# Optimization experiments

Measured on AMD Instinct MI355X. Metric: run time of the kernel, lower is better.

The kernel has to match this reference:

```python
import jax, jax.numpy as jnp
import numpy as np
import math

REG = 0.1      # entropic regularization (self.reg)
TEMP = 0.1     # self.temperature from kwargs
ITERS = 20     # self.iters
EPS = 1e-5     # torch LayerNorm eps
ALPHA_BOTH = -100.0


def _layernorm(t, g, b):
    mu = jnp.mean(t, axis=-1, keepdims=True)
    var = jnp.mean((t - mu) ** 2, axis=-1, keepdims=True)
    return (t - mu) / jnp.sqrt(var + EPS) * g + b


def setup_inputs() -> dict:
    key = jax.random.key(0)
    k1, k2, k3 = jax.random.split(key, 3)
    B, M, N, H = 2048, 36, 36, 768
    x = jax.random.normal(k1, (B, M, H), jnp.float32)
    y = jax.random.normal(k2, (B, N, H), jnp.float32)
    # dustbin scorer params: LayerNorm(H) -> Linear(H, 1)
    ln_g = jnp.ones((H,), jnp.float32)
    ln_b = jnp.zeros((H,), jnp.float32)
    w = jax.random.normal(k3, (H, 1), jnp.float32) * (1.0 / math.sqrt(H))
    b_lin = jnp.zeros((1,), jnp.float32)
    return {"x": x, "y": y, "ln_g": ln_g, "ln_b": ln_b, "w": w, "b_lin": b_lin}


def reference(x, y, ln_g, ln_b, w, b_lin):
    B, M, H = x.shape
    N = y.shape[1]
    # CosineScorer(temperature=1).score(x, y, get_diag=False)
    xn = x / jnp.linalg.norm(x, axis=-1, keepdims=True)
    yn = y / jnp.linalg.norm(y, axis=-1, keepdims=True)
    scores = jnp.einsum('bmh,bnh->bmn', xn, yn)            # (B, M, N)
    # tanh-clipped learned dustbin scores
    ax = jnp.tanh(_layernorm(x, ln_g, ln_b) @ w + b_lin)   # (B, M, 1)
    ay = jnp.tanh(_layernorm(y, ln_g, ln_b) @ w + b_lin)   # (B, N, 1)
    # augmented score matrix with dustbin row/col
    alpha_both = jnp.full((B, 1, 1), ALPHA_BOTH, scores.dtype)
    top = jnp.concatenate([scores, ax], axis=2)                       # (B, M, N+1)
    bot = jnp.concatenate([jnp.swapaxes(ay, 1, 2), alpha_both], axis=2)  # (B, 1, N+1)
    couplings = jnp.concatenate([top, bot], axis=1) / REG             # (B, M+1, N+1)
    # SuperGlue-style marginals: dustbins absorb the complementary mass
    norm_c = -math.log(M + N)
    log_mu = jnp.concatenate([jnp.full((M,), norm_c),
                              jnp.array([math.log(N) + norm_c])]).astype(scores.dtype)
    log_nu = jnp.concatenate([jnp.full((N,), norm_c),
                              jnp.array([math.log(M) + norm_c])]).astype(scores.dtype)

    def body(carry, _):
        u, v = carry
        u = log_mu[None, :] - jax.nn.logsumexp(couplings + v[:, None, :], axis=2)
        v = log_nu[None, :] - jax.nn.logsumexp(couplings + u[:, :, None], axis=1)
        return (u, v), None

    u0 = jnp.zeros((B, M + 1), scores.dtype)
    v0 = jnp.zeros((B, N + 1), scores.dtype)
    (u, v), _ = jax.lax.scan(body, (u0, v0), None, length=ITERS)
    Z = couplings + u[:, :, None] + v[:, None, :] - norm_c            # log matching, (B, M+1, N+1)
    # scalar alignment score per batch element: <P, S> / temperature
    total = jnp.sum(jnp.exp(Z[:, :-1, :-1]) * scores, axis=(1, 2)) / TEMP
    return Z, total
```

## Files before the change

kernel.cpp:

```cpp
#include <hip/hip_runtime.h>
#include <stdint.h>
#include <stddef.h>


typedef float  f4  __attribute__((ext_vector_type(4)));
typedef short  s8v __attribute__((ext_vector_type(8)));
typedef unsigned int u2v __attribute__((ext_vector_type(2)));

#define HD   768
#define MR   36
#define KC   128
#define NCH  6
#define AS   136
#define CS   44
#define LOG2E 1.4426950408889634f
#define LN2   0.6931471805599453f
#define L272  6.169925001442312f
#define KC2   (10.0f*LOG2E)
#define NEGB  (-1.0e30f)

__device__ __forceinline__ uint32_t pkbf2(float a, float b) {
    uint32_t ua = __float_as_uint(a), ub = __float_as_uint(b);
    ua += 0x7FFFu + ((ua >> 16) & 1u);
    ub += 0x7FFFu + ((ub >> 16) & 1u);
    return (ua >> 16) | (ub & 0xFFFF0000u);
}

__global__ __launch_bounds__(256, 3) void sinkhorn_kernel(
    const float* __restrict__ X, const float* __restrict__ Y,
    const float* __restrict__ LG, const float* __restrict__ LB,
    const float* __restrict__ W,  const float* __restrict__ BL,
    float* __restrict__ OUT, int NB)
{
    __shared__ __align__(16) uint16_t Al[48 * AS];
    __shared__ __align__(16) uint16_t Bt[48 * AS];
    __shared__ __align__(16) float C2 [37 * CS];
    __shared__ __align__(16) float C2T[37 * CS];
    __shared__ __align__(16) float u_l[40];
    __shared__ __align__(16) float v_l[40];
    __shared__ float stx[MR * 3], sty[MR * 3];
    __shared__ float rnx[MR], rny[MR];
    __shared__ float s_gw, s_bw, red[4];

    const int t  = threadIdx.x;
    const int b  = blockIdx.x;
    const int wv = t >> 6, ln = t & 63;
    const int c4 = t & 31, gg = t >> 5;

    if (t < 40) { u_l[t] = 0.0f; v_l[t] = 0.0f; }
    if (t < 37) {
        C2 [t * CS + 37] = NEGB; C2 [t * CS + 38] = NEGB; C2 [t * CS + 39] = NEGB;
        C2T[t * CS + 37] = NEGB; C2T[t * CS + 38] = NEGB; C2T[t * CS + 39] = NEGB;
    }
    if (wv == 3) {
        float a = 0.0f, c = 0.0f;
        for (int q = 0; q < 12; ++q) {
            int h = ln + 64 * q;
            float wval = W[h];
            a += LG[h] * wval; c += LB[h] * wval;
        }
        for (int o = 32; o > 0; o >>= 1) { a += __shfl_down(a, o); c += __shfl_down(c, o); }
        if (ln == 0) { s_gw = a; s_bw = c; }
    }

    float sx[5][3], sy[5][3];
    #pragma unroll
    for (int p = 0; p < 5; ++p)
        #pragma unroll
        for (int s = 0; s < 3; ++s) { sx[p][s] = 0.0f; sy[p][s] = 0.0f; }

    f4 acc[3];
    #pragma unroll
    for (int i = 0; i < 3; ++i) acc[i] = (f4){0.0f, 0.0f, 0.0f, 0.0f};

    const float* xb = X + (size_t)b * (MR * HD);
    const float* yb = Y + (size_t)b * (MR * HD);

    const int frow = ln & 15, fq = ln >> 4;
    const int rA = (wv * 16 + frow) * AS + fq * 8;

    for (int kc = 0; kc < NCH; ++kc) {
        const int k0 = kc * KC;
        f4 gv = *(const f4*)(LG + k0 + c4 * 4);
        f4 wvec = *(const f4*)(W + k0 + c4 * 4);
        f4 gw = gv * wvec;
        #pragma unroll
        for (int p = 0; p < 5; ++p) {
            if (p < 4 || t < 128) {
                const int row = (p < 4) ? (p * 8 + gg) : (32 + gg);
                f4 xv = *(const f4*)(xb + row * HD + k0 + c4 * 4);
                sx[p][0] += (xv.x + xv.y) + (xv.z + xv.w);
                sx[p][1] += xv.x * xv.x + xv.y * xv.y + xv.z * xv.z + xv.w * xv.w;
                sx[p][2] += xv.x * gw.x + xv.y * gw.y + xv.z * gw.z + xv.w * gw.w;
                u2v px; px.x = pkbf2(xv.x, xv.y); px.y = pkbf2(xv.z, xv.w);
                *(u2v*)&Al[row * AS + c4 * 4] = px;
                f4 yv = *(const f4*)(yb + row * HD + k0 + c4 * 4);
                sy[p][0] += (yv.x + yv.y) + (yv.z + yv.w);
                sy[p][1] += yv.x * yv.x + yv.y * yv.y + yv.z * yv.z + yv.w * yv.w;
                sy[p][2] += yv.x * gw.x + yv.y * gw.y + yv.z * gw.z + yv.w * gw.w;
                u2v py; py.x = pkbf2(yv.x, yv.y); py.y = pkbf2(yv.z, yv.w);
                *(u2v*)&Bt[row * AS + c4 * 4] = py;
            }
        }
        __syncthreads();
        if (wv < 3) {
            #pragma unroll
            for (int ks = 0; ks < 4; ++ks) {
                s8v af = *(const s8v*)&Al[rA + ks * 32];
                #pragma unroll
                for (int tn = 0; tn < 3; ++tn) {
                    s8v bf = *(const s8v*)&Bt[(tn * 16 + frow) * AS + fq * 8 + ks * 32];
                    acc[tn] = __builtin_amdgcn_mfma_f32_16x16x32_bf16(af, bf, acc[tn], 0, 0, 0);
                }
            }
        }
        __syncthreads();
    }

    #pragma unroll
    for (int p = 0; p < 5; ++p) {
        const int row = (p < 4) ? (p * 8 + gg) : (32 + gg);
        #pragma unroll
        for (int s = 0; s < 3; ++s) {
            float a = sx[p][s], c = sy[p][s];
            for (int o = 16; o > 0; o >>= 1) { a += __shfl_down(a, o, 32); c += __shfl_down(c, o, 32); }
            if ((t & 31) == 0 && row < MR) { stx[row * 3 + s] = a; sty[row * 3 + s] = c; }
        }
    }
    __syncthreads();

    {
        const float blin = BL[0];
        if (t < MR) {
            float Sx = stx[t * 3], Sxx = stx[t * 3 + 1], Sxw = stx[t * 3 + 2];
            rnx[t] = __builtin_amdgcn_rsqf(Sxx);
            float mu  = Sx * (1.0f / HD);
            float var = Sxx * (1.0f / HD) - mu * mu;
            float rsd = __builtin_amdgcn_rsqf(var + 1e-5f);
            float lin = (Sxw - mu * s_gw) * rsd + s_bw + blin;
            float e   = __builtin_amdgcn_exp2f(2.0f * LOG2E * lin);
            float th  = (e - 1.0f) / (e + 1.0f);
            C2 [t * CS + 36] = th * KC2;
            C2T[36 * CS + t] = th * KC2;
        } else if (t >= 64 && t < 64 + MR) {
            int j = t - 64;
            float Sy = sty[j * 3], Syy = sty[j * 3 + 1], Syw = sty[j * 3 + 2];
            rny[j] = __builtin_amdgcn_rsqf(Syy);
            float mu  = Sy * (1.0f / HD);
            float var = Syy * (1.0f / HD) - mu * mu;
            float rsd = __builtin_amdgcn_rsqf(var + 1e-5f);
            float lin = (Syw - mu * s_gw) * rsd + s_bw + blin;
            float e   = __builtin_amdgcn_exp2f(2.0f * LOG2E * lin);
            float th  = (e - 1.0f) / (e + 1.0f);
            C2 [36 * CS + j] = th * KC2;
            C2T[j * CS + 36] = th * KC2;
        } else if (t == 128) {
            C2 [36 * CS + 36] = -100.0f * KC2;
            C2T[36 * CS + 36] = -100.0f * KC2;
        }
    }
    __syncthreads();

    if (wv < 3) {
        #pragma unroll
        for (int tn = 0; tn < 3; ++tn) {
            #pragma unroll
            for (int r = 0; r < 4; ++r) {
                int i = wv * 16 + fq * 4 + r;
                int j = tn * 16 + frow;
                if (i < MR && j < MR) {
                    float v = acc[tn][r] * rnx[i] * rny[j] * KC2;
                    C2 [i * CS + j] = v;
                    C2T[j * CS + i] = v;
                }
            }
        }
    }
    __syncthreads();

    if (wv == 0 && ln < 37) {
        const int i = ln;
        const float lmu = (i < MR) ? -L272 : -1.0f;
        f4 cr[10], ct[10];
        #pragma unroll
        for (int jj = 0; jj < 10; ++jj) {
            cr[jj] = *(const f4*)(&C2 [i * CS + jj * 4]);
            ct[jj] = *(const f4*)(&C2T[i * CS + jj * 4]);
        }
        for (int it = 0; it < 20; ++it) {
            float tt[40];
            float m = -3.0e38f;
            #pragma unroll
            for (int jj = 0; jj < 10; ++jj) {
                f4 vv = *(const f4*)(&v_l[jj * 4]);
                f4 s = cr[jj] + vv;
                tt[jj*4+0] = s.x; tt[jj*4+1] = s.y; tt[jj*4+2] = s.z; tt[jj*4+3] = s.w;
                m = fmaxf(m, fmaxf(fmaxf(s.x, s.y), fmaxf(s.z, s.w)));
            }
            float ss = 0.0f;
            #pragma unroll
            for (int jj = 0; jj < 10; ++jj)
                ss += __builtin_amdgcn_exp2f(tt[jj*4+0] - m) + __builtin_amdgcn_exp2f(tt[jj*4+1] - m)
                    + __builtin_amdgcn_exp2f(tt[jj*4+2] - m) + __builtin_amdgcn_exp2f(tt[jj*4+3] - m);
            u_l[i] = lmu - (m + __builtin_amdgcn_logf(ss));
            m = -3.0e38f;
            #pragma unroll
            for (int jj = 0; jj < 10; ++jj) {
                f4 uu = *(const f4*)(&u_l[jj * 4]);
                f4 s = ct[jj] + uu;
                tt[jj*4+0] = s.x; tt[jj*4+1] = s.y; tt[jj*4+2] = s.z; tt[jj*4+3] = s.w;
                m = fmaxf(m, fmaxf(fmaxf(s.x, s.y), fmaxf(s.z, s.w)));
            }
            ss = 0.0f;
            #pragma unroll
            for (int jj = 0; jj < 10; ++jj)
                ss += __builtin_amdgcn_exp2f(tt[jj*4+0] - m) + __builtin_amdgcn_exp2f(tt[jj*4+1] - m)
                    + __builtin_amdgcn_exp2f(tt[jj*4+2] - m) + __builtin_amdgcn_exp2f(tt[jj*4+3] - m);
            v_l[i] = lmu - (m + __builtin_amdgcn_logf(ss));
        }
    }
    __syncthreads();

    float tot = 0.0f;
    const size_t ob = (size_t)b * 1369;
    for (int e = t; e < 1369; e += 256) {
        int i = e / 37, j = e - i * 37;
        float c2v = C2[i * CS + j];
        float z2  = c2v + u_l[i] + v_l[j] + L272;
        OUT[ob + e] = z2 * LN2;
        if (i < MR && j < MR)
            tot += __builtin_amdgcn_exp2f(z2) * (c2v * (0.1f * LN2));
    }
    for (int o = 32; o > 0; o >>= 1) tot += __shfl_down(tot, o);
    if (ln == 0) red[wv] = tot;
    __syncthreads();
    if (t == 0) OUT[(size_t)NB * 1369 + b] = (red[0] + red[1] + red[2] + red[3]) * 10.0f;
}

extern "C" void kernel_launch(void* const* d_in, const int* in_sizes, int n_in,
                              void* d_out, int out_size, void* d_ws, size_t ws_size,
                              hipStream_t stream) {
    const float* X  = (const float*)d_in[0];
    const float* Y  = (const float*)d_in[1];
    const float* LG = (const float*)d_in[2];
    const float* LB = (const float*)d_in[3];
    const float* W  = (const float*)d_in[4];
    const float* BL = (const float*)d_in[5];
    const int NB = in_sizes[0] / (MR * HD);
    hipLaunchKernelGGL(sinkhorn_kernel, dim3(NB), dim3(256), 0, stream,
                       X, Y, LG, LB, W, BL, (float*)d_out, NB);
}
```

Measured before the change: 518.7 us.

## Alias transposed score buffer onto GEMM staging LDS and raise occupancy to 5 blocks

Merges the bf16 A/B staging buffers into one 72-row region and reuses it for the transposed coupling matrix after the GEMM. This cuts LDS per block so the launch bound can go from 3 to 5 blocks per CU. The Sinkhorn loop now reads couplings from LDS each iteration instead of holding 80 registers, uses split max and sum accumulators for more ILP, and rotates which wavefront runs it by block index. Clamped row indices keep the MFMA reads of padded rows inside the smaller buffer, and the extra LDS reads per iteration add latency to the serial loop.

Measured after the change: 635.1 us. +22.4%, slower.

```diff
diff --git a/kernel.cpp b/kernel.cpp
--- a/kernel.cpp
+++ b/kernel.cpp
@@ -13,6 +13,7 @@
 #define NCH  6
 #define AS   136
 #define CS   44
+#define ITERS 20
 #define LOG2E 1.4426950408889634f
 #define LN2   0.6931471805599453f
 #define L272  6.169925001442312f
@@ -26,22 +27,31 @@
     return (ua >> 16) | (ub & 0xFFFF0000u);
 }
 
-__global__ __launch_bounds__(256, 3) void sinkhorn_kernel(
+__device__ __forceinline__ f4 fmax4(f4 a, f4 b) {
+    f4 r;
+    r.x = fmaxf(a.x, b.x); r.y = fmaxf(a.y, b.y);
+    r.z = fmaxf(a.z, b.z); r.w = fmaxf(a.w, b.w);
+    return r;
+}
+
+__global__ __launch_bounds__(256, 5) void sinkhorn_kernel(
     const float* __restrict__ X, const float* __restrict__ Y,
     const float* __restrict__ LG, const float* __restrict__ LB,
     const float* __restrict__ W,  const float* __restrict__ BL,
     float* __restrict__ OUT, int NB)
 {
-    __shared__ __align__(16) uint16_t Al[48 * AS];
-    __shared__ __align__(16) uint16_t Bt[48 * AS];
+    __shared__ __align__(16) uint16_t AB[72 * AS];
     __shared__ __align__(16) float C2 [37 * CS];
-    __shared__ __align__(16) float C2T[37 * CS];
     __shared__ __align__(16) float u_l[40];
     __shared__ __align__(16) float v_l[40];
     __shared__ float stx[MR * 3], sty[MR * 3];
     __shared__ float rnx[MR], rny[MR];
     __shared__ float s_gw, s_bw, red[4];
 
+    uint16_t* Al = AB;
+    uint16_t* Bt = AB + 36 * AS;
+    float*    C2T = (float*)AB;
+
     const int t  = threadIdx.x;
     const int b  = blockIdx.x;
     const int wv = t >> 6, ln = t & 63;
@@ -49,8 +59,7 @@
 
     if (t < 40) { u_l[t] = 0.0f; v_l[t] = 0.0f; }
     if (t < 37) {
-        C2 [t * CS + 37] = NEGB; C2 [t * CS + 38] = NEGB; C2 [t * CS + 39] = NEGB;
-        C2T[t * CS + 37] = NEGB; C2T[t * CS + 38] = NEGB; C2T[t * CS + 39] = NEGB;
+        C2[t * CS + 37] = NEGB; C2[t * CS + 38] = NEGB; C2[t * CS + 39] = NEGB;
     }
     if (wv == 3) {
         float a = 0.0f, c = 0.0f;
@@ -77,7 +86,12 @@
     const float* yb = Y + (size_t)b * (MR * HD);
 
     const int frow = ln & 15, fq = ln >> 4;
-    const int rA = (wv * 16 + frow) * AS + fq * 8;
+    const int arR = wv * 16 + frow;
+    const int rA  = ((arR < MR) ? arR : (MR - 1)) * AS + fq * 8;
+    const int rB0 = (frow)      * AS + fq * 8;
+    const int rB1 = (16 + frow) * AS + fq * 8;
+    const int bt2 = 32 + frow;
+    const int rB2 = ((bt2 < MR) ? bt2 : (MR - 1)) * AS + fq * 8;
 
     for (int kc = 0; kc < NCH; ++kc) {
         const int k0 = kc * KC;
@@ -107,11 +121,12 @@
             #pragma unroll
             for (int ks = 0; ks < 4; ++ks) {
                 s8v af = *(const s8v*)&Al[rA + ks * 32];
-                #pragma unroll
-                for (int tn = 0; tn < 3; ++tn) {
-                    s8v bf = *(const s8v*)&Bt[(tn * 16 + frow) * AS + fq * 8 + ks * 32];
-                    acc[tn] = __builtin_amdgcn_mfma_f32_16x16x32_bf16(af, bf, acc[tn], 0, 0, 0);
-                }
+                s8v b0 = *(const s8v*)&Bt[rB0 + ks * 32];
+                acc[0] = __builtin_amdgcn_mfma_f32_16x16x32_bf16(af, b0, acc[0], 0, 0, 0);
+                s8v b1 = *(const s8v*)&Bt[rB1 + ks * 32];
+                acc[1] = __builtin_amdgcn_mfma_f32_16x16x32_bf16(af, b1, acc[1], 0, 0, 0);
+                s8v b2 = *(const s8v*)&Bt[rB2 + ks * 32];
+                acc[2] = __builtin_amdgcn_mfma_f32_16x16x32_bf16(af, b2, acc[2], 0, 0, 0);
             }
         }
         __syncthreads();
@@ -157,6 +172,9 @@
         } else if (t == 128) {
             C2 [36 * CS + 36] = -100.0f * KC2;
             C2T[36 * CS + 36] = -100.0f * KC2;
+        } else if (t >= 192 && t < 192 + 37) {
+            int r = t - 192;
+            C2T[r * CS + 37] = NEGB; C2T[r * CS + 38] = NEGB; C2T[r * CS + 39] = NEGB;
         }
     }
     __syncthreads();
@@ -178,45 +196,66 @@
     }
     __syncthreads();
 
-    if (wv == 0 && ln < 37) {
+    if (wv == (b & 3) && ln < 37) {
         const int i = ln;
         const float lmu = (i < MR) ? -L272 : -1.0f;
-        f4 cr[10], ct[10];
-        #pragma unroll
-        for (int jj = 0; jj < 10; ++jj) {
-            cr[jj] = *(const f4*)(&C2 [i * CS + jj * 4]);
-            ct[jj] = *(const f4*)(&C2T[i * CS + jj * 4]);
-        }
-        for (int it = 0; it < 20; ++it) {
-            float tt[40];
-            float m = -3.0e38f;
-            #pragma unroll
-            for (int jj = 0; jj < 10; ++jj) {
-                f4 vv = *(const f4*)(&v_l[jj * 4]);
-                f4 s = cr[jj] + vv;
-                tt[jj*4+0] = s.x; tt[jj*4+1] = s.y; tt[jj*4+2] = s.z; tt[jj*4+3] = s.w;
-                m = fmaxf(m, fmaxf(fmaxf(s.x, s.y), fmaxf(s.z, s.w)));
-            }
-            float ss = 0.0f;
-            #pragma unroll
-            for (int jj = 0; jj < 10; ++jj)
-                ss += __builtin_amdgcn_exp2f(tt[jj*4+0] - m) + __builtin_amdgcn_exp2f(tt[jj*4+1] - m)
-                    + __builtin_amdgcn_exp2f(tt[jj*4+2] - m) + __builtin_amdgcn_exp2f(tt[jj*4+3] - m);
-            u_l[i] = lmu - (m + __builtin_amdgcn_logf(ss));
-            m = -3.0e38f;
-            #pragma unroll
-            for (int jj = 0; jj < 10; ++jj) {
-                f4 uu = *(const f4*)(&u_l[jj * 4]);
-                f4 s = ct[jj] + uu;
-                tt[jj*4+0] = s.x; tt[jj*4+1] = s.y; tt[jj*4+2] = s.z; tt[jj*4+3] = s.w;
-                m = fmaxf(m, fmaxf(fmaxf(s.x, s.y), fmaxf(s.z, s.w)));
-            }
-            ss = 0.0f;
-            #pragma unroll
-            for (int jj = 0; jj < 10; ++jj)
-                ss += __builtin_amdgcn_exp2f(tt[jj*4+0] - m) + __builtin_amdgcn_exp2f(tt[jj*4+1] - m)
-                    + __builtin_amdgcn_exp2f(tt[jj*4+2] - m) + __builtin_amdgcn_exp2f(tt[jj*4+3] - m);
-            v_l[i] = lmu - (m + __builtin_amdgcn_logf(ss));
+        const float* Cr = C2  + i * CS;
+        const float* Ct = C2T + i * CS;
+        for (int it = 0; it < ITERS; ++it) {
+            {
+                f4 s[10], ma, mb;
+                #pragma unroll
+                for (int jj = 0; jj < 10; ++jj) {
+                    f4 sv = *(const f4*)(Cr + jj * 4) + *(const f4*)(&v_l[jj * 4]);
+                    s[jj] = sv;
+                    if (jj == 0) ma = sv;
+                    else if (jj == 1) mb = sv;
+                    else if (jj & 1) mb = fmax4(mb, sv);
+                    else ma = fmax4(ma, sv);
+                }
+                f4 mm = fmax4(ma, mb);
+                float m = fmaxf(fmaxf(mm.x, mm.y), fmaxf(mm.z, mm.w));
+                f4 ea = (f4){0.0f,0.0f,0.0f,0.0f}, eb = (f4){0.0f,0.0f,0.0f,0.0f};
+                #pragma unroll
+                for (int jj = 0; jj < 10; ++jj) {
+                    f4 sv = s[jj], ev;
+                    ev.x = __builtin_amdgcn_exp2f(sv.x - m);
+                    ev.y = __builtin_amdgcn_exp2f(sv.y - m);
+                    ev.z = __builtin_amdgcn_exp2f(sv.z - m);
+                    ev.w = __builtin_amdgcn_exp2f(sv.w - m);
+                    if (jj & 1) eb += ev; else ea += ev;
+                }
+                f4 et = ea + eb;
+                float ss = (et.x + et.y) + (et.z + et.w);
+                u_l[i] = lmu - (m + __builtin_amdgcn_logf(ss));
+            }
+            {
+                f4 s[10], ma, mb;
+                #pragma unroll
+                for (int jj = 0; jj < 10; ++jj) {
+                    f4 sv = *(const f4*)(Ct + jj * 4) + *(const f4*)(&u_l[jj * 4]);
+                    s[jj] = sv;
+                    if (jj == 0) ma = sv;
+                    else if (jj == 1) mb = sv;
+                    else if (jj & 1) mb = fmax4(mb, sv);
+                    else ma = fmax4(ma, sv);
+                }
+                f4 mm = fmax4(ma, mb);
+                float m = fmaxf(fmaxf(mm.x, mm.y), fmaxf(mm.z, mm.w));
+                f4 ea = (f4){0.0f,0.0f,0.0f,0.0f}, eb = (f4){0.0f,0.0f,0.0f,0.0f};
+                #pragma unroll
+                for (int jj = 0; jj < 10; ++jj) {
+                    f4 sv = s[jj], ev;
+                    ev.x = __builtin_amdgcn_exp2f(sv.x - m);
+                    ev.y = __builtin_amdgcn_exp2f(sv.y - m);
+                    ev.z = __builtin_amdgcn_exp2f(sv.z - m);
+                    ev.w = __builtin_amdgcn_exp2f(sv.w - m);
+                    if (jj & 1) eb += ev; else ea += ev;
+                }
+                f4 et = ea + eb;
+                float ss = (et.x + et.y) + (et.z + et.w);
+                v_l[i] = lmu - (m + __builtin_amdgcn_logf(ss));
+            }
         }
     }
     __syncthreads();
```
